# Optimization experiments

Measured on AMD Instinct MI355X. Metric: run time of the kernel, lower is better.

Reference implementation:

```python
import jax, jax.numpy as jnp
import numpy as np

EPS = 1e-5
ALPHA = 1.0

def _conv1x1(x, w, b):
    # x: [N,C,T,V], w: [O,C], b: [O] -> [N,O,T,V]
    return jnp.einsum('nctv,oc->notv', x, w) + b[None, :, None, None]

def _groupnorm1(x, gamma, beta):
    # GroupNorm(1, C): normalize over (C,T,V) per sample
    mu = jnp.mean(x, axis=(1, 2, 3), keepdims=True)
    var = jnp.var(x, axis=(1, 2, 3), keepdims=True)
    xn = (x - mu) * jax.lax.rsqrt(var + EPS)
    return xn * gamma[None, :, None, None] + beta[None, :, None, None]

def setup_inputs() -> dict:
    key = jax.random.key(0)
    ks = jax.random.split(key, 12)
    N, Cin, T, V, O, R = 128, 64, 128, 25, 64, 8
    s_in = 1.0 / np.sqrt(Cin)
    s_r = 1.0 / np.sqrt(R)
    return {
        'x':  jax.random.normal(ks[0], (N, Cin, T, V), jnp.float32),
        'A':  jax.random.normal(ks[1], (V, V), jnp.float32) * 0.1,
        'w1': jax.random.normal(ks[2], (R, Cin), jnp.float32) * s_in,
        'b1': jnp.zeros((R,), jnp.float32),
        'g1': jnp.ones((R,), jnp.float32),
        'be1': jnp.zeros((R,), jnp.float32),
        'w2': jax.random.normal(ks[3], (R, Cin), jnp.float32) * s_in,
        'b2': jnp.zeros((R,), jnp.float32),
        'g2': jnp.ones((R,), jnp.float32),
        'be2': jnp.zeros((R,), jnp.float32),
        'w3': jax.random.normal(ks[4], (O, Cin), jnp.float32) * s_in,
        'b3': jnp.zeros((O,), jnp.float32),
        'w4': jax.random.normal(ks[5], (O, R), jnp.float32) * s_r,
        'b4': jnp.zeros((O,), jnp.float32),
    }

def reference(x, A, w1, b1, g1, be1, w2, b2, g2, be2, w3, b3, w4, b4):
    # branch 1: conv1 -> GroupNorm -> temporal mean -> pairwise diff -> tanh
    x1 = _groupnorm1(_conv1x1(x, w1, b1), g1, be1).mean(axis=2)      # [N,R,V]
    y1 = jnp.tanh(x1[..., :, None] - x1[..., None, :])               # [N,R,V,V]
    # branch 2: conv2 -> GroupNorm -> temporal mean -> outer product -> tanh
    x2 = _groupnorm1(_conv1x1(x, w2, b2), g2, be2).mean(axis=2)      # [N,R,V]
    y2 = jnp.tanh(x2[..., :, None] * x2[..., None, :])               # [N,R,V,V]
    # value branch
    x3 = _conv1x1(x, w3, b3)                                          # [N,O,T,V]
    # dynamic adjacency: conv4 over rel channels
    ys = y1 + ALPHA * y2 + A[None, None]                              # [N,R,V,V]
    y_sum = jnp.einsum('nruv,or->nouv', ys, w4) + b4[None, :, None, None]
    # aggregation over vertices
    y = jnp.einsum('ncuv,nctv->nctu', y_sum, x3)                      # [N,O,T,V]
    return y
```

## Files before the change

### kernel.cpp

```cpp
#include <hip/hip_runtime.h>

#define EPSV 1e-5f
constexpr int NN = 128, CIN = 64, TT = 128, VV = 25, OO = 64, RR = 8;
constexpr int TVQ   = TT * VV;
constexpr int XSAMP = CIN * TVQ;
constexpr int YSAMP = OO * TT * VV;
constexpr int RTV   = RR * TT * VV;
constexpr int S12N  = 2 * RR * VV;
constexpr int YS2_SAMP = VV * OO * 28;
constexpr int X3_SAMP  = TVQ * OO;

__global__ __launch_bounds__(256) void kZero(float* __restrict__ p, int n)
{
    int i = blockIdx.x * 256 + threadIdx.x;
    if (i < n) p[i] = 0.f;
}

__global__ __launch_bounds__(256) void kA(const float* __restrict__ x,
    const float* __restrict__ w1, const float* __restrict__ b1,
    const float* __restrict__ w2, const float* __restrict__ b2,
    float* __restrict__ s12g, float* __restrict__ ssqg)
{
    __shared__ float wt1[CIN * RR], wt2[CIN * RR];
    __shared__ float s1l[RR * VV], s2l[RR * VV];
    __shared__ float redA[4], redB[4];
    const int tid = threadIdx.x;
    const int tc  = blockIdx.x;
    const int n   = blockIdx.y;

    for (int e = tid; e < CIN * RR; e += 256) {
        int r = e >> 6, c = e & 63;
        wt1[c * RR + r] = w1[e];
        wt2[c * RR + r] = w2[e];
    }
    for (int e = tid; e < 2 * RR * VV; e += 256) {
        if (e < RR * VV) s1l[e] = 0.f; else s2l[e - RR * VV] = 0.f;
    }
    __syncthreads();

    float acc1[4][RR], acc2[4][RR];
    #pragma unroll
    for (int j = 0; j < 4; ++j)
        #pragma unroll
        for (int r = 0; r < RR; ++r) { acc1[j][r] = 0.f; acc2[j][r] = 0.f; }

    const bool active = (tid < 200);
    const int p0 = tid * 4;
    const float* xb = x + (size_t)n * XSAMP + tc * 800 + p0;
    if (active) {
        #pragma unroll 4
        for (int c = 0; c < CIN; ++c) {
            float4 xv  = *(const float4*)(xb + c * TVQ);
            float4 wa1 = *(const float4*)(&wt1[c * RR]);
            float4 wb1 = *(const float4*)(&wt1[c * RR + 4]);
            float4 wa2 = *(const float4*)(&wt2[c * RR]);
            float4 wb2 = *(const float4*)(&wt2[c * RR + 4]);
            float xj[4]  = {xv.x, xv.y, xv.z, xv.w};
            float w1v[8] = {wa1.x, wa1.y, wa1.z, wa1.w, wb1.x, wb1.y, wb1.z, wb1.w};
            float w2v[8] = {wa2.x, wa2.y, wa2.z, wa2.w, wb2.x, wb2.y, wb2.z, wb2.w};
            #pragma unroll
            for (int j = 0; j < 4; ++j)
                #pragma unroll
                for (int r = 0; r < RR; ++r) {
                    acc1[j][r] += w1v[r] * xj[j];
                    acc2[j][r] += w2v[r] * xj[j];
                }
        }
    }

    float b1r[RR], b2r[RR];
    #pragma unroll
    for (int r = 0; r < RR; ++r) { b1r[r] = b1[r]; b2r[r] = b2[r]; }

    float ssq1 = 0.f, ssq2 = 0.f;
    if (active) {
        #pragma unroll
        for (int j = 0; j < 4; ++j) {
            int v = (p0 + j) % VV;
            #pragma unroll
            for (int r = 0; r < RR; ++r) {
                float c1 = acc1[j][r] + b1r[r]; ssq1 += c1 * c1;
                float c2 = acc2[j][r] + b2r[r]; ssq2 += c2 * c2;
                atomicAdd(&s1l[r * VV + v], acc1[j][r]);
                atomicAdd(&s2l[r * VV + v], acc2[j][r]);
            }
        }
    }
    #pragma unroll
    for (int off = 32; off > 0; off >>= 1) {
        ssq1 += __shfl_down(ssq1, off);
        ssq2 += __shfl_down(ssq2, off);
    }
    if ((tid & 63) == 0) { redA[tid >> 6] = ssq1; redB[tid >> 6] = ssq2; }
    __syncthreads();
    for (int e = tid; e < S12N; e += 256) {
        float pv = (e < RR * VV) ? s1l[e] : s2l[e - RR * VV];
        atomicAdd(&s12g[n * S12N + e], pv);
    }
    if (tid == 0) {
        atomicAdd(&ssqg[n * 2 + 0], redA[0] + redA[1] + redA[2] + redA[3]);
        atomicAdd(&ssqg[n * 2 + 1], redB[0] + redB[1] + redB[2] + redB[3]);
    }
}

__device__ __forceinline__ float tanh_fast(float v)
{
    float e = __expf(2.f * v);
    return 1.f - 2.f / (e + 1.f);
}

__global__ __launch_bounds__(512) void kB(
    const float* __restrict__ s12g, const float* __restrict__ ssqg,
    const float* __restrict__ b1, const float* __restrict__ g1, const float* __restrict__ be1,
    const float* __restrict__ b2, const float* __restrict__ g2, const float* __restrict__ be2,
    const float* __restrict__ Amat, const float* __restrict__ w4, const float* __restrict__ b4,
    float* __restrict__ ys2)
{
    __shared__ float x1g[RR * VV], x2g[RR * VV];
    __shared__ float w4t[RR * OO];
    __shared__ float b4l[OO];
    __shared__ float ysl[625 * 9];
    __shared__ float stats[2];
    __shared__ float mss[4];
    const int tid = threadIdx.x;
    const int n   = blockIdx.x;

    if (tid < 2) stats[tid] = 0.f;
    if (tid < OO * RR) {
        int o = tid >> 3, r = tid & 7;
        w4t[r * OO + o] = w4[tid];
    }
    if (tid < OO) b4l[tid] = b4[tid];
    __syncthreads();

    float sv = 0.f;
    if (tid < S12N) {
        sv = s12g[n * S12N + tid];
        atomicAdd(&stats[tid / (RR * VV)], sv);
    }
    __syncthreads();
    if (tid == 0) {
        float sb1 = 0.f, sb2 = 0.f;
        for (int r = 0; r < RR; ++r) { sb1 += b1[r]; sb2 += b2[r]; }
        float mu1 = (stats[0] + (float)(TT * VV) * sb1) / (float)RTV;
        float mu2 = (stats[1] + (float)(TT * VV) * sb2) / (float)RTV;
        float var1 = ssqg[n * 2 + 0] / (float)RTV - mu1 * mu1;
        float var2 = ssqg[n * 2 + 1] / (float)RTV - mu2 * mu2;
        mss[0] = mu1; mss[1] = rsqrtf(var1 + EPSV);
        mss[2] = mu2; mss[3] = rsqrtf(var2 + EPSV);
    }
    __syncthreads();
    if (tid < S12N) {
        int br = tid / (RR * VV);
        int i  = tid % (RR * VV);
        int r  = i / VV;
        float mu = mss[br * 2], rs = mss[br * 2 + 1];
        float mean_t = sv / (float)TT + (br ? b2[r] : b1[r]);
        float g  = br ? g2[r]  : g1[r];
        float be = br ? be2[r] : be1[r];
        float val = g * (mean_t - mu) * rs + be;
        if (br == 0) x1g[i] = val; else x2g[i] = val;
    }
    __syncthreads();

    for (int p = tid; p < 625; p += 512) {
        int u = p / VV, v = p % VV;
        float Av = Amat[p];
        #pragma unroll
        for (int r = 0; r < RR; ++r) {
            float d = x1g[r * VV + u] - x1g[r * VV + v];
            float m = x2g[r * VV + u] * x2g[r * VV + v];
            ysl[p * 9 + r] = tanh_fast(d) + tanh_fast(m) + Av;
        }
    }
    __syncthreads();

    float* yn = ys2 + (size_t)n * YS2_SAMP;
    for (int e4 = tid; e4 < 11200; e4 += 512) {
        int u   = e4 / 448;
        int rem = e4 - u * 448;
        int o   = rem / 7;
        int v4  = (rem - o * 7) * 4;
        float w[RR];
        #pragma unroll
        for (int r = 0; r < RR; ++r) w[r] = w4t[r * OO + o];
        const float bb = b4l[o];
        float4 out;
        float* op = &out.x;
        #pragma unroll
        for (int j = 0; j < 4; ++j) {
            int v = v4 + j;
            float a = 0.f;
            if (v < VV) {
                a = bb;
                const float* yr = &ysl[(u * VV + v) * 9];
                #pragma unroll
                for (int r = 0; r < RR; ++r) a += w[r] * yr[r];
            }
            op[j] = a;
        }
        *(float4*)(yn + u * (OO * 28) + o * 28 + v4) = out;
    }
}

__global__ __launch_bounds__(256) void kC1(const float* __restrict__ x,
    const float* __restrict__ w3, const float* __restrict__ b3,
    float* __restrict__ x3T)
{
    __shared__ float wt[CIN * 68];
    const int tid = threadIdx.x;
    const int n   = blockIdx.y;
    const int oq  = tid & 7;
    const int pg  = tid >> 3;
    const int p0  = blockIdx.x * 256 + pg * 8;

    for (int e = tid; e < CIN * OO; e += 256) {
        int o = e >> 6, c = e & 63;
        wt[c * 68 + o] = w3[e];
    }
    __syncthreads();

    float acc[8][8];
    #pragma unroll
    for (int i = 0; i < 8; ++i)
        #pragma unroll
        for (int j = 0; j < 8; ++j) acc[i][j] = 0.f;

    const bool act = (p0 < TVQ);
    const float* xp = x + (size_t)n * XSAMP + p0;
    if (act) {
        #pragma unroll 4
        for (int c = 0; c < CIN; ++c) {
            const float* xc = xp + c * TVQ;
            float4 xa = *(const float4*)(xc);
            float4 xb = *(const float4*)(xc + 4);
            const float* wr = &wt[c * 68 + oq * 8];
            float4 wa = *(const float4*)(wr);
            float4 wb = *(const float4*)(wr + 4);
            float xv[8] = {xa.x, xa.y, xa.z, xa.w, xb.x, xb.y, xb.z, xb.w};
            float wv[8] = {wa.x, wa.y, wa.z, wa.w, wb.x, wb.y, wb.z, wb.w};
            #pragma unroll
            for (int i = 0; i < 8; ++i)
                #pragma unroll
                for (int j = 0; j < 8; ++j)
                    acc[i][j] += wv[i] * xv[j];
        }
    }

    float bo[8];
    #pragma unroll
    for (int i = 0; i < 8; ++i) bo[i] = b3[oq * 8 + i];
    if (act) {
        float* dst = x3T + (size_t)n * X3_SAMP + (size_t)p0 * OO + oq * 8;
        #pragma unroll
        for (int j = 0; j < 8; ++j) {
            float4 s0, s1;
            s0.x = acc[0][j] + bo[0]; s0.y = acc[1][j] + bo[1];
            s0.z = acc[2][j] + bo[2]; s0.w = acc[3][j] + bo[3];
            s1.x = acc[4][j] + bo[4]; s1.y = acc[5][j] + bo[5];
            s1.z = acc[6][j] + bo[6]; s1.w = acc[7][j] + bo[7];
            *(float4*)(dst + j * OO)     = s0;
            *(float4*)(dst + j * OO + 4) = s1;
        }
    }
}

__global__ __launch_bounds__(256) void kC2(const float* __restrict__ x3T,
    const float* __restrict__ ys2, float* __restrict__ y)
{
    __shared__ float lds[OO * 101];
    const int tid = threadIdx.x;
    const int tc  = blockIdx.x;
    const int n   = blockIdx.y;
    const int t0  = tc * 8;
    const int o2  = tid & 63;
    const int th2 = tid >> 6;

    const float* xb = x3T + (size_t)n * X3_SAMP;
    float acc2[2][28];
    #pragma unroll
    for (int row = 0; row < 2; ++row) {
        const int t = t0 + 2 * th2 + row;
        #pragma unroll
        for (int v = 0; v < VV; ++v)
            acc2[row][v] = xb[(size_t)(t * VV + v) * OO + o2];
        acc2[row][25] = 0.f; acc2[row][26] = 0.f; acc2[row][27] = 0.f;
    }

    const float* yo = ys2 + (size_t)n * YS2_SAMP + o2 * 28;
    float res[2][VV];
    #pragma unroll
    for (int u = 0; u < VV; ++u) {
        const float* yu = yo + u * (OO * 28);
        float r0 = 0.f, r1 = 0.f;
        #pragma unroll
        for (int v4 = 0; v4 < 28; v4 += 4) {
            float4 w = *(const float4*)(yu + v4);
            r0 += w.x * acc2[0][v4]     + w.y * acc2[0][v4 + 1]
                + w.z * acc2[0][v4 + 2] + w.w * acc2[0][v4 + 3];
            r1 += w.x * acc2[1][v4]     + w.y * acc2[1][v4 + 1]
                + w.z * acc2[1][v4 + 2] + w.w * acc2[1][v4 + 3];
        }
        res[0][u] = r0;
        res[1][u] = r1;
    }

    float* yb = y + (size_t)n * YSAMP + t0 * VV;
    #pragma unroll 1
    for (int half = 0; half < 2; ++half) {
        __syncthreads();
        if ((th2 >> 1) == half) {
            #pragma unroll
            for (int row = 0; row < 2; ++row) {
                const int tl = (2 * th2 + row) & 3;
                #pragma unroll
                for (int u = 0; u < VV; ++u)
                    lds[o2 * 101 + tl * VV + u] = res[row][u];
            }
        }
        __syncthreads();
        for (int e = tid; e < 6400; e += 256) {
            int o = e / 100, m = e % 100;
            yb[o * TVQ + half * 100 + m] = lds[o * 101 + m];
        }
    }
}

__global__ __launch_bounds__(256) void kC(
    const float* __restrict__ x, const float* __restrict__ w3,
    const float* __restrict__ b3, const float* __restrict__ ys2,
    float* __restrict__ y)
{
    __shared__ float lds[7168];
    const int tid = threadIdx.x;
    const int tc  = blockIdx.x;
    const int n   = blockIdx.y;
    const int t0  = tc * 8;

    const int og = tid >> 3;
    const int th = tid & 7;
    const int o0 = og * 2;

    float acc[2][VV];
    #pragma unroll
    for (int j = 0; j < 2; ++j)
        #pragma unroll
        for (int v = 0; v < VV; ++v) acc[j][v] = 0.f;

    const float* xn = x + (size_t)n * XSAMP + t0 * VV;
    #pragma unroll 1
    for (int cpass = 0; cpass < 2; ++cpass) {
        __syncthreads();
        for (int e4 = tid; e4 < 32 * 50; e4 += 256) {
            int cl = e4 / 50, r4 = (e4 % 50) * 4;
            float4 tv = *(const float4*)(xn + (cpass * 32 + cl) * TVQ + r4);
            float a[4] = {tv.x, tv.y, tv.z, tv.w};
            #pragma unroll
            for (int j = 0; j < 4; ++j) {
                int rem = r4 + j;
                lds[cl * 224 + (rem / VV) * 28 + (rem % VV)] = a[j];
            }
        }
        __syncthreads();
        #pragma unroll 1
        for (int q = 0; q < 2; ++q) {
            float w3q[2][16];
            #pragma unroll
            for (int j = 0; j < 2; ++j)
                #pragma unroll
                for (int k4 = 0; k4 < 4; ++k4) {
                    float4 wv = *(const float4*)(w3 + (o0 + j) * CIN
                                                 + cpass * 32 + q * 16 + k4 * 4);
                    w3q[j][k4*4+0] = wv.x; w3q[j][k4*4+1] = wv.y;
                    w3q[j][k4*4+2] = wv.z; w3q[j][k4*4+3] = wv.w;
                }
            #pragma unroll
            for (int ci = 0; ci < 16; ++ci) {
                const float* p = &lds[(q * 16 + ci) * 224 + th * 28];
                float4 a0 = *(const float4*)(p + 0);
                float4 a1 = *(const float4*)(p + 4);
                float4 a2 = *(const float4*)(p + 8);
                float4 a3 = *(const float4*)(p + 12);
                float4 a4 = *(const float4*)(p + 16);
                float4 a5 = *(const float4*)(p + 20);
                float  a6 = p[24];
                #pragma unroll
                for (int j = 0; j < 2; ++j) {
                    const float w = w3q[j][ci];
                    float* a = acc[j];
                    a[0]  += w*a0.x; a[1]  += w*a0.y; a[2]  += w*a0.z; a[3]  += w*a0.w;
                    a[4]  += w*a1.x; a[5]  += w*a1.y; a[6]  += w*a1.z; a[7]  += w*a1.w;
                    a[8]  += w*a2.x; a[9]  += w*a2.y; a[10] += w*a2.z; a[11] += w*a2.w;
                    a[12] += w*a3.x; a[13] += w*a3.y; a[14] += w*a3.z; a[15] += w*a3.w;
                    a[16] += w*a4.x; a[17] += w*a4.y; a[18] += w*a4.z; a[19] += w*a4.w;
                    a[20] += w*a5.x; a[21] += w*a5.y; a[22] += w*a5.z; a[23] += w*a5.w;
                    a[24] += w*a6;
                }
            }
        }
    }

    const int o2  = tid & 63;
    const int th2 = tid >> 6;
    const float bias = b3[o2];
    float acc2[2][VV];

    #pragma unroll 1
    for (int half = 0; half < 2; ++half) {
        __syncthreads();
        if ((th >> 2) == half) {
            const int tl = th & 3;
            #pragma unroll
            for (int j = 0; j < 2; ++j)
                #pragma unroll
                for (int v = 0; v < VV; ++v)
                    lds[tl * 1601 + (o0 + j) * VV + v] = acc[j][v];
        }
        __syncthreads();
        if ((th2 >> 1) == half) {
            #pragma unroll
            for (int row = 0; row < 2; ++row) {
                const int tl = (2 * th2 + row) & 3;
                #pragma unroll
                for (int v = 0; v < VV; ++v)
                    acc2[row][v] = lds[tl * 1601 + o2 * VV + v];
            }
        }
    }
    #pragma unroll
    for (int row = 0; row < 2; ++row)
        #pragma unroll
        for (int v = 0; v < VV; ++v) acc2[row][v] += bias;

    const float* yT = ys2 + (size_t)n * YS2_SAMP + o2 * 28;
    float res[2][VV];
    #pragma unroll
    for (int u = 0; u < VV; ++u) {
        float r0 = 0.f, r1 = 0.f;
        #pragma unroll
        for (int v = 0; v < VV; ++v) {
            float yv = yT[u * (OO * 28) + v];
            r0 += yv * acc2[0][v];
            r1 += yv * acc2[1][v];
        }
        res[0][u] = r0;
        res[1][u] = r1;
    }

    float* yb = y + (size_t)n * YSAMP + t0 * VV;
    #pragma unroll 1
    for (int half = 0; half < 2; ++half) {
        __syncthreads();
        if ((th2 >> 1) == half) {
            #pragma unroll
            for (int row = 0; row < 2; ++row) {
                const int tl = (2 * th2 + row) & 3;
                #pragma unroll
                for (int u = 0; u < VV; ++u)
                    lds[o2 * 101 + tl * VV + u] = res[row][u];
            }
        }
        __syncthreads();
        for (int e = tid; e < 6400; e += 256) {
            int o = e / 100, m = e % 100;
            yb[o * TVQ + half * 100 + m] = lds[o * 101 + m];
        }
    }
}

extern "C" void kernel_launch(void* const* d_in, const int* in_sizes, int n_in,
                              void* d_out, int out_size, void* d_ws, size_t ws_size,
                              hipStream_t stream)
{
    const float* x   = (const float*)d_in[0];
    const float* Am  = (const float*)d_in[1];
    const float* w1  = (const float*)d_in[2];
    const float* b1  = (const float*)d_in[3];
    const float* g1  = (const float*)d_in[4];
    const float* be1 = (const float*)d_in[5];
    const float* w2  = (const float*)d_in[6];
    const float* b2  = (const float*)d_in[7];
    const float* g2  = (const float*)d_in[8];
    const float* be2 = (const float*)d_in[9];
    const float* w3  = (const float*)d_in[10];
    const float* b3  = (const float*)d_in[11];
    const float* w4  = (const float*)d_in[12];
    const float* b4  = (const float*)d_in[13];
    float* y  = (float*)d_out;
    float* ws = (float*)d_ws;
    float* s12g = ws;
    float* ssqg = s12g + (size_t)NN * S12N;
    float* ys2  = ssqg + (size_t)NN * 2;
    float* x3T  = ys2 + (size_t)NN * YS2_SAMP;

    const int nz = NN * S12N + NN * 2;
    hipLaunchKernelGGL(kZero, dim3((nz + 255) / 256), dim3(256), 0, stream, ws, nz);
    hipLaunchKernelGGL(kA, dim3(4, NN), dim3(256), 0, stream,
                       x, w1, b1, w2, b2, s12g, ssqg);
    hipLaunchKernelGGL(kB, dim3(NN), dim3(512), 0, stream,
                       s12g, ssqg, b1, g1, be1, b2, g2, be2, Am, w4, b4, ys2);

    const size_t baseF = (size_t)NN * S12N + NN * 2 + (size_t)NN * YS2_SAMP;
    const size_t wsF   = ws_size / sizeof(float);
    long availF = (long)wsF - (long)baseF;
    int chunk = 0;
    if (availF >= (long)X3_SAMP) {
        long c = availF / (long)X3_SAMP;
        chunk = (c > NN) ? NN : (int)c;
    }
    if (chunk >= 1) {
        for (int n0 = 0; n0 < NN; n0 += chunk) {
            int nc = (NN - n0 < chunk) ? (NN - n0) : chunk;
            hipLaunchKernelGGL(kC1, dim3(13, nc), dim3(256), 0, stream,
                               x + (size_t)n0 * XSAMP, w3, b3, x3T);
            hipLaunchKernelGGL(kC2, dim3(16, nc), dim3(256), 0, stream,
                               x3T, ys2 + (size_t)n0 * YS2_SAMP,
                               y + (size_t)n0 * YSAMP);
        }
    } else {
        hipLaunchKernelGGL(kC, dim3(16, NN), dim3(256), 0, stream,
                           x, w3, b3, ys2, y);
    }
}
```

Measured before the change: 453.9 us.

## Split kB across vertex blocks and interleave ys layout for coalesced kC2 reads

kB now launches 5 blocks per sample, each handling 5 rows u of the adjacency, instead of one block per sample. This spreads the small tanh/conv4 stage across more CUs. The ys output layout changes from [u][o][28] to [u][v4][o][4], so kC2's per-thread float4 loads across o are contiguous across lanes, giving coalesced global reads. The cost is that each kB block redundantly recomputes the per-sample statistics and x1/x2 vectors.

```diff
diff --git a/kernel.cpp b/kernel.cpp
--- a/kernel.cpp
+++ b/kernel.cpp
@@ -7,7 +7,7 @@
 constexpr int YSAMP = OO * TT * VV;
 constexpr int RTV   = RR * TT * VV;
 constexpr int S12N  = 2 * RR * VV;
-constexpr int YS2_SAMP = VV * OO * 28;
+constexpr int YS3_SAMP = VV * 7 * OO * 4;
 constexpr int X3_SAMP  = TVQ * OO;
 
 __global__ __launch_bounds__(256) void kZero(float* __restrict__ p, int n)
@@ -114,16 +114,17 @@
     const float* __restrict__ b1, const float* __restrict__ g1, const float* __restrict__ be1,
     const float* __restrict__ b2, const float* __restrict__ g2, const float* __restrict__ be2,
     const float* __restrict__ Amat, const float* __restrict__ w4, const float* __restrict__ b4,
-    float* __restrict__ ys2)
+    float* __restrict__ ys3)
 {
     __shared__ float x1g[RR * VV], x2g[RR * VV];
     __shared__ float w4t[RR * OO];
     __shared__ float b4l[OO];
-    __shared__ float ysl[625 * 9];
+    __shared__ float ysl[125 * 9];
     __shared__ float stats[2];
     __shared__ float mss[4];
     const int tid = threadIdx.x;
-    const int n   = blockIdx.x;
+    const int ub0 = blockIdx.x * 5;
+    const int n   = blockIdx.y;
 
     if (tid < 2) stats[tid] = 0.f;
     if (tid < OO * RR) {
@@ -163,9 +164,9 @@
     }
     __syncthreads();
 
-    for (int p = tid; p < 625; p += 512) {
-        int u = p / VV, v = p % VV;
-        float Av = Amat[p];
+    for (int p = tid; p < 125; p += 512) {
+        int u = ub0 + p / VV, v = p % VV;
+        float Av = Amat[u * VV + v];
         #pragma unroll
         for (int r = 0; r < RR; ++r) {
             float d = x1g[r * VV + u] - x1g[r * VV + v];
@@ -175,12 +176,12 @@
     }
     __syncthreads();
 
-    float* yn = ys2 + (size_t)n * YS2_SAMP;
-    for (int e4 = tid; e4 < 11200; e4 += 512) {
-        int u   = e4 / 448;
-        int rem = e4 - u * 448;
-        int o   = rem / 7;
-        int v4  = (rem - o * 7) * 4;
+    float* yn = ys3 + (size_t)n * YS3_SAMP + ub0 * (7 * OO * 4);
+    for (int e4 = tid; e4 < 2240; e4 += 512) {
+        int ul  = e4 / 448;
+        int rem = e4 - ul * 448;
+        int v4  = rem >> 6;
+        int o   = rem & 63;
         float w[RR];
         #pragma unroll
         for (int r = 0; r < RR; ++r) w[r] = w4t[r * OO + o];
@@ -189,17 +190,17 @@
         float* op = &out.x;
         #pragma unroll
         for (int j = 0; j < 4; ++j) {
-            int v = v4 + j;
+            int v = v4 * 4 + j;
             float a = 0.f;
             if (v < VV) {
                 a = bb;
-                const float* yr = &ysl[(u * VV + v) * 9];
+                const float* yr = &ysl[(ul * VV + v) * 9];
                 #pragma unroll
                 for (int r = 0; r < RR; ++r) a += w[r] * yr[r];
             }
             op[j] = a;
         }
-        *(float4*)(yn + u * (OO * 28) + o * 28 + v4) = out;
+        *(float4*)(yn + (size_t)e4 * 4) = out;
     }
 }
 
@@ -266,7 +267,7 @@
 }
 
 __global__ __launch_bounds__(256) void kC2(const float* __restrict__ x3T,
-    const float* __restrict__ ys2, float* __restrict__ y)
+    const float* __restrict__ ys3, float* __restrict__ y)
 {
     __shared__ float lds[OO * 101];
     const int tid = threadIdx.x;
@@ -287,19 +288,19 @@
         acc2[row][25] = 0.f; acc2[row][26] = 0.f; acc2[row][27] = 0.f;
     }
 
-    const float* yo = ys2 + (size_t)n * YS2_SAMP + o2 * 28;
+    const float* yo = ys3 + (size_t)n * YS3_SAMP + o2 * 4;
     float res[2][VV];
     #pragma unroll
     for (int u = 0; u < VV; ++u) {
-        const float* yu = yo + u * (OO * 28);
+        const float* yu = yo + u * (7 * OO * 4);
         float r0 = 0.f, r1 = 0.f;
         #pragma unroll
-        for (int v4 = 0; v4 < 28; v4 += 4) {
-            float4 w = *(const float4*)(yu + v4);
-            r0 += w.x * acc2[0][v4]     + w.y * acc2[0][v4 + 1]
-                + w.z * acc2[0][v4 + 2] + w.w * acc2[0][v4 + 3];
-            r1 += w.x * acc2[1][v4]     + w.y * acc2[1][v4 + 1]
-                + w.z * acc2[1][v4 + 2] + w.w * acc2[1][v4 + 3];
+        for (int v4 = 0; v4 < 7; ++v4) {
+            float4 w = *(const float4*)(yu + v4 * (OO * 4));
+            r0 += w.x * acc2[0][v4*4]     + w.y * acc2[0][v4*4 + 1]
+                + w.z * acc2[0][v4*4 + 2] + w.w * acc2[0][v4*4 + 3];
+            r1 += w.x * acc2[1][v4*4]     + w.y * acc2[1][v4*4 + 1]
+                + w.z * acc2[1][v4*4 + 2] + w.w * acc2[1][v4*4 + 3];
         }
         res[0][u] = r0;
         res[1][u] = r1;
@@ -328,7 +329,7 @@
 
 __global__ __launch_bounds__(256) void kC(
     const float* __restrict__ x, const float* __restrict__ w3,
-    const float* __restrict__ b3, const float* __restrict__ ys2,
+    const float* __restrict__ b3, const float* __restrict__ ys3,
     float* __restrict__ y)
 {
     __shared__ float lds[7168];
@@ -432,14 +433,14 @@
         #pragma unroll
         for (int v = 0; v < VV; ++v) acc2[row][v] += bias;
 
-    const float* yT = ys2 + (size_t)n * YS2_SAMP + o2 * 28;
+    const float* yT = ys3 + (size_t)n * YS3_SAMP + o2 * 4;
     float res[2][VV];
     #pragma unroll
     for (int u = 0; u < VV; ++u) {
         float r0 = 0.f, r1 = 0.f;
         #pragma unroll
         for (int v = 0; v < VV; ++v) {
-            float yv = yT[u * (OO * 28) + v];
+            float yv = yT[u * (7 * OO * 4) + (v >> 2) * (OO * 4) + (v & 3)];
             r0 += yv * acc2[0][v];
             r1 += yv * acc2[1][v];
         }
@@ -490,17 +491,17 @@
     float* ws = (float*)d_ws;
     float* s12g = ws;
     float* ssqg = s12g + (size_t)NN * S12N;
-    float* ys2  = ssqg + (size_t)NN * 2;
-    float* x3T  = ys2 + (size_t)NN * YS2_SAMP;
+    float* ys3  = ssqg + (size_t)NN * 2;
+    float* x3T  = ys3 + (size_t)NN * YS3_SAMP;
 
     const int nz = NN * S12N + NN * 2;
     hipLaunchKernelGGL(kZero, dim3((nz + 255) / 256), dim3(256), 0, stream, ws, nz);
     hipLaunchKernelGGL(kA, dim3(4, NN), dim3(256), 0, stream,
                        x, w1, b1, w2, b2, s12g, ssqg);
-    hipLaunchKernelGGL(kB, dim3(NN), dim3(512), 0, stream,
-                       s12g, ssqg, b1, g1, be1, b2, g2, be2, Am, w4, b4, ys2);
-
-    const size_t baseF = (size_t)NN * S12N + NN * 2 + (size_t)NN * YS2_SAMP;
+    hipLaunchKernelGGL(kB, dim3(5, NN), dim3(512), 0, stream,
+                       s12g, ssqg, b1, g1, be1, b2, g2, be2, Am, w4, b4, ys3);
+
+    const size_t baseF = (size_t)NN * S12N + NN * 2 + (size_t)NN * YS3_SAMP;
     const size_t wsF   = ws_size / sizeof(float);
     long availF = (long)wsF - (long)baseF;
     int chunk = 0;
@@ -514,11 +515,11 @@
             hipLaunchKernelGGL(kC1, dim3(13, nc), dim3(256), 0, stream,
                                x + (size_t)n0 * XSAMP, w3, b3, x3T);
             hipLaunchKernelGGL(kC2, dim3(16, nc), dim3(256), 0, stream,
-                               x3T, ys2 + (size_t)n0 * YS2_SAMP,
+                               x3T, ys3 + (size_t)n0 * YS3_SAMP,
                                y + (size_t)n0 * YSAMP);
         }
     } else {
         hipLaunchKernelGGL(kC, dim3(16, NN), dim3(256), 0, stream,
-                           x, w3, b3, ys2, y);
-    }
-}
+                           x, w3, b3, ys3, y);
+    }
+}
```

Measured after the change: 444.2 us. 2.1% less time.
